# Optimization experiments

Measured on AMD Instinct MI355X. Metric: run time of the kernel, lower is better.

Reference implementation:

```python
import jax, jax.numpy as jnp
import numpy as np

N_HEADS = 8
STATE_TEMP = 0.5


def layer_norm(x, g, b, eps=1e-5):
    m = x.mean(-1, keepdims=True)
    v = ((x - m) ** 2).mean(-1, keepdims=True)
    return (x - m) / jnp.sqrt(v + eps) * g + b


def setup_inputs() -> dict:
    key = jax.random.key(0)
    ks = jax.random.split(key, 16)
    B, G, H, C, S, M, L = 2048, 10000, 256, 16, 32, 100, 3
    f32 = jnp.float32
    rn = lambda k, shape, scale: jax.random.normal(k, shape, f32) * scale
    return {
        'x': rn(ks[0], (B, G), 1.0),
        'enc_w1': rn(ks[1], (G, 2 * H), 1.0 / np.sqrt(G)),
        'enc_b1': jnp.zeros((2 * H,), f32),
        'enc_ln_g': jnp.ones((2 * H,), f32),
        'enc_ln_b': jnp.zeros((2 * H,), f32),
        'enc_w2': rn(ks[2], (2 * H, H), 1.0 / np.sqrt(2 * H)),
        'enc_b2': jnp.zeros((H,), f32),
        'mod_assign': rn(ks[3], (M, G), 1.0),
        'mod_inter': rn(ks[4], (M, M), 0.1) + jnp.eye(M, dtype=f32),
        'qkv_w': rn(ks[5], (L, H, 3 * H), 1.0 / np.sqrt(H)),
        'qkv_b': jnp.zeros((L, 3 * H), f32),
        'out_w': rn(ks[6], (L, H, H), 1.0 / np.sqrt(H)),
        'out_b': jnp.zeros((L, H), f32),
        'ln_g': jnp.ones((L, H), f32),
        'ln_b': jnp.zeros((L, H), f32),
        'prototypes': rn(ks[7], (S, H), 1.0),
        'clf_w1': rn(ks[8], (H, H // 2), 1.0 / np.sqrt(H)),
        'clf_b1': jnp.zeros((H // 2,), f32),
        'clf_w2': rn(ks[9], (H // 2, C), 1.0 / np.sqrt(H // 2)),
        'clf_b2': jnp.zeros((C,), f32),
        'marker_weights': jax.random.uniform(ks[10], (C, G), f32),
    }


def reference(x, enc_w1, enc_b1, enc_ln_g, enc_ln_b, enc_w2, enc_b2,
              mod_assign, mod_inter, qkv_w, qkv_b, out_w, out_b, ln_g, ln_b,
              prototypes, clf_w1, clf_b1, clf_w2, clf_b2, marker_weights):
    B = x.shape[0]
    Hd = enc_w2.shape[1]
    hd = Hd // N_HEADS
    # --- gene encoder (Linear -> LN -> ReLU -> Linear), dropout off (eval) ---
    h = jax.nn.relu(layer_norm(x @ enc_w1 + enc_b1, enc_ln_g, enc_ln_b))
    gene_features = h @ enc_w2 + enc_b2  # [B, Hd]
    # --- gene regulatory module (only sparsity_loss feeds the output dict) ---
    module_weights = jax.nn.softmax(mod_assign, axis=1)  # [M, G]
    sparsity_loss = jnp.mean(jnp.abs(module_weights)) * 0.01
    # --- stacked biological attention over seq_len N = 1 ---
    f = gene_features[:, None, :]  # [B, 1, Hd]
    for i in range(qkv_w.shape[0]):
        residual = f
        qkv = (f @ qkv_w[i] + qkv_b[i]).reshape(B, 1, 3, N_HEADS, hd)
        qkv = qkv.transpose(2, 0, 3, 1, 4)  # [3, B, nh, 1, hd]
        q, k, v = qkv[0], qkv[1], qkv[2]
        # N=1 != n_genes so the interaction-mask branch is skipped
        attn = jax.nn.softmax((q @ k.swapaxes(-2, -1)) * hd ** -0.5, axis=-1)
        o = (attn @ v).swapaxes(1, 2).reshape(B, 1, Hd)
        o = o @ out_w[i] + out_b[i]
        f = layer_norm(o + residual, ln_g[i], ln_b[i])
    feats = f[:, 0]  # [B, Hd]
    # --- soft assignment to cell-state prototypes via cosine similarity ---
    fn = jnp.linalg.norm(feats, axis=-1, keepdims=True)  # [B, 1]
    pn = jnp.linalg.norm(prototypes, axis=-1)            # [S]
    sim = (feats @ prototypes.T) / jnp.maximum(fn * pn[None, :], 1e-8)
    state_weights = jax.nn.softmax(sim / STATE_TEMP, axis=1)
    cell_states = state_weights @ prototypes  # [B, Hd]
    # --- classifier head ---
    logits = jax.nn.relu(cell_states @ clf_w1 + clf_b1) @ clf_w2 + clf_b2
    # --- eval-mode marker scores from buffer ---
    C, G = marker_weights.shape
    marker_scores = jnp.broadcast_to(marker_weights[None], (B, C, G))
    denom = jnp.maximum(jnp.sum(jnp.abs(marker_weights), axis=1, keepdims=True), 1e-12)
    marker_importance = marker_weights / denom
    return (logits, cell_states, sparsity_loss, marker_scores, marker_importance)
```

## Files before the change

### kernel.cpp

```cpp
#include <hip/hip_runtime.h>
#include <stdint.h>

#define GG 10000
#define H2 512
#define KP 10240
#define KCH 1280
#define KSTEPS 40

#define O_CS 32768L
#define O_SP 557056L
#define O_MS 557057L
#define O_MI 328237057L

typedef __attribute__((ext_vector_type(8))) short v8s;
typedef __attribute__((ext_vector_type(4))) float v4f;
typedef __attribute__((ext_vector_type(4))) unsigned short u16x4;
typedef __attribute__((ext_vector_type(8))) unsigned short u16x8;

__device__ __forceinline__ unsigned short bf16_rne(float f){
  unsigned u = __float_as_uint(f);
  u += 0x7fffu + ((u>>16)&1u);
  return (unsigned short)(u>>16);
}
__device__ __forceinline__ float bf16_f(unsigned short h){
  return __uint_as_float(((unsigned)h)<<16);
}

#define GL16(g,l) __builtin_amdgcn_global_load_lds( \
    (__attribute__((address_space(1))) void*)(uintptr_t)(g), \
    (__attribute__((address_space(3))) void*)(l), 16, 0, 0)

__global__ __launch_bounds__(256) void k_split_x(const float* __restrict__ x,
    unsigned short* __restrict__ xh){
  int idx = blockIdx.x*256 + threadIdx.x;
  int row = idx / (KP/4);
  int k = (idx - row*(KP/4))*4;
  float4 v = make_float4(0.f,0.f,0.f,0.f);
  if (k < GG) v = *(const float4*)(x + (long)row*GG + k);
  float c[4] = {v.x,v.y,v.z,v.w};
  u16x4 hv;
  #pragma unroll
  for (int j=0;j<4;j++) hv[j] = bf16_rne(c[j]);
  *(u16x4*)(xh + (long)row*KP + k) = hv;
}

__global__ __launch_bounds__(256) void k_split_w1t(const float* __restrict__ w1,
    unsigned short* __restrict__ wth, unsigned short* __restrict__ wtl){
  __shared__ unsigned T[64][65];
  int k0 = blockIdx.x*64, n0 = blockIdx.y*64;
  int tid = threadIdx.x;
  {
    int kr = tid>>2, nc = (tid&3)*16;
    int kk = k0 + kr;
    #pragma unroll
    for (int j=0;j<16;j+=4){
      float4 v = make_float4(0.f,0.f,0.f,0.f);
      if (kk < GG) v = *(const float4*)(w1 + (long)kk*H2 + n0 + nc + j);
      float c[4] = {v.x,v.y,v.z,v.w};
      #pragma unroll
      for (int jj=0;jj<4;jj++){
        unsigned short h = bf16_rne(c[jj]);
        unsigned short l = bf16_rne(c[jj] - bf16_f(h));
        T[kr][nc+j+jj] = (unsigned)h | ((unsigned)l<<16);
      }
    }
  }
  __syncthreads();
  {
    int n = tid>>2, kc = (tid&3)*16;
    u16x8 h0, h1, l0, l1;
    #pragma unroll
    for (int j=0;j<8;j++){
      unsigned a = T[kc+j][n];
      unsigned b = T[kc+8+j][n];
      h0[j] = (unsigned short)(a & 0xffffu); l0[j] = (unsigned short)(a>>16);
      h1[j] = (unsigned short)(b & 0xffffu); l1[j] = (unsigned short)(b>>16);
    }
    long off = (long)(n0+n)*KP + k0 + kc;
    *(u16x8*)(wth+off)   = h0; *(u16x8*)(wth+off+8) = h1;
    *(u16x8*)(wtl+off)   = l0; *(u16x8*)(wtl+off+8) = l1;
  }
}

__global__ __launch_bounds__(256) void k_gemm1(
    const unsigned short* __restrict__ xh,
    const unsigned short* __restrict__ wth, const unsigned short* __restrict__ wtl,
    float* __restrict__ pc){
  __shared__ unsigned short Ah[4096], Bh[4096], Bl[4096];
  const int tid = threadIdx.x;
  const int wid = tid>>6, lane = tid&63;
  const int bm = blockIdx.x, bn = blockIdx.y, kz = blockIdx.z;
  const int c0 = wid*2, c1 = c0+1;
  const int srow = lane>>2;
  const int sk8 = (lane&3)*8;
  const long kb0 = (long)kz*KCH + sk8;
  const long rA0 = (long)(bm*128 + c0*16 + srow)*KP + kb0;
  const long rA1 = (long)(bm*128 + c1*16 + srow)*KP + kb0;
  const long rB0 = (long)(bn*128 + c0*16 + srow)*KP + kb0;
  const long rB1 = (long)(bn*128 + c1*16 + srow)*KP + kb0;
  const unsigned short* pAh0 = xh + rA0;  const unsigned short* pAh1 = xh + rA1;
  const unsigned short* pBh0 = wth + rB0; const unsigned short* pBh1 = wth + rB1;
  const unsigned short* pBl0 = wtl + rB0; const unsigned short* pBl1 = wtl + rB1;
  unsigned short* dAh0 = &Ah[c0*512]; unsigned short* dAh1 = &Ah[c1*512];
  unsigned short* dBh0 = &Bh[c0*512]; unsigned short* dBh1 = &Bh[c1*512];
  unsigned short* dBl0 = &Bl[c0*512]; unsigned short* dBl1 = &Bl[c1*512];
  const int wr = wid>>1, wc = wid&1;
  const int fr = lane&15, fq = lane>>4;
  v4f acc[4][4];
  #pragma unroll
  for (int m=0;m<4;m++)
    #pragma unroll
    for (int n=0;n<4;n++){ v4f z = {0.f,0.f,0.f,0.f}; acc[m][n] = z; }

  for (int s=0; s<KSTEPS; ++s){
    GL16(pAh0, dAh0); GL16(pAh1, dAh1);
    GL16(pBh0, dBh0); GL16(pBh1, dBh1);
    GL16(pBl0, dBl0); GL16(pBl1, dBl1);
    pAh0 += 32; pAh1 += 32;
    pBh0 += 32; pBh1 += 32; pBl0 += 32; pBl1 += 32;
    __syncthreads();
    v8s ah[4], bh[4], bl[4];
    #pragma unroll
    for (int m=0;m<4;m++)
      ah[m] = *(const v8s*)&Ah[(wr*64 + m*16 + fr)*32 + fq*8];
    #pragma unroll
    for (int n=0;n<4;n++){
      int off = (wc*64 + n*16 + fr)*32 + fq*8;
      bh[n] = *(const v8s*)&Bh[off];
      bl[n] = *(const v8s*)&Bl[off];
    }
    #pragma unroll
    for (int m=0;m<4;m++)
      #pragma unroll
      for (int n=0;n<4;n++){
        acc[m][n] = __builtin_amdgcn_mfma_f32_16x16x32_bf16(ah[m], bh[n], acc[m][n], 0,0,0);
        acc[m][n] = __builtin_amdgcn_mfma_f32_16x16x32_bf16(ah[m], bl[n], acc[m][n], 0,0,0);
      }
    __syncthreads();
  }
  float* op = pc + (long)kz*(2048L*512L);
  #pragma unroll
  for (int m=0;m<4;m++){
    #pragma unroll
    for (int n=0;n<4;n++){
      int col = bn*128 + wc*64 + n*16 + fr;
      #pragma unroll
      for (int r=0;r<4;r++){
        int row = bm*128 + wr*64 + m*16 + fq*4 + r;
        op[(long)row*512 + col] = acc[m][n][r];
      }
    }
  }
}

__global__ __launch_bounds__(256) void k_reduce_ln(const float* __restrict__ pc,
    const float* __restrict__ b1, const float* __restrict__ g, const float* __restrict__ b,
    float* __restrict__ t1){
  __shared__ float red[8];
  int row = blockIdx.x, tid = threadIdx.x;
  long base = (long)row*512;
  float v0 = b1[tid], v1 = b1[tid+256];
  #pragma unroll
  for (int kz=0;kz<8;kz++){
    v0 += pc[(long)kz*1048576 + base + tid];
    v1 += pc[(long)kz*1048576 + base + tid + 256];
  }
  float s = v0+v1, q = v0*v0 + v1*v1;
  #pragma unroll
  for (int off=32; off; off>>=1){ s += __shfl_xor(s, off); q += __shfl_xor(q, off); }
  if ((tid&63)==0){ red[tid>>6] = s; red[4+(tid>>6)] = q; }
  __syncthreads();
  float sum = red[0]+red[1]+red[2]+red[3];
  float ssq = red[4]+red[5]+red[6]+red[7];
  float mean = sum*(1.f/512.f);
  float var  = ssq*(1.f/512.f) - mean*mean;
  float rstd = rsqrtf(var + 1e-5f);
  float r0 = (v0-mean)*rstd*g[tid]     + b[tid];
  float r1 = (v1-mean)*rstd*g[tid+256] + b[tid+256];
  t1[base+tid]     = fmaxf(r0, 0.f);
  t1[base+tid+256] = fmaxf(r1, 0.f);
}

__global__ __launch_bounds__(256) void k_gemm_f32(
    const float* __restrict__ A, int lda,
    const float* __restrict__ W, int ldw,
    const float* __restrict__ bias,
    float* __restrict__ C, int ldo, int K){
  __shared__ float As[64][36];
  __shared__ float WsT[64][36];
  const int tid = threadIdx.x;
  const int bx = blockIdx.x, by = blockIdx.y;
  const int tx = tid&15, ty = tid>>4;
  const int ar = tid>>2, ak = (tid&3)*8;
  const int wr2 = tid>>3, wc2 = (tid&7)*8;
  float acc[4][4];
  #pragma unroll
  for (int i=0;i<4;i++)
    #pragma unroll
    for (int j=0;j<4;j++) acc[i][j] = 0.f;
  for (int kb=0; kb<K; kb+=32){
    float4 a0 = *(const float4*)(A + (long)(bx*64+ar)*lda + kb + ak);
    float4 a1 = *(const float4*)(A + (long)(bx*64+ar)*lda + kb + ak + 4);
    float4 w0 = *(const float4*)(W + (long)(kb+wr2)*ldw + by*64 + wc2);
    float4 w1v= *(const float4*)(W + (long)(kb+wr2)*ldw + by*64 + wc2 + 4);
    __syncthreads();
    *(float4*)&As[ar][ak]   = a0;
    *(float4*)&As[ar][ak+4] = a1;
    float cw[8] = {w0.x,w0.y,w0.z,w0.w,w1v.x,w1v.y,w1v.z,w1v.w};
    #pragma unroll
    for (int jj=0;jj<8;jj++) WsT[wc2+jj][wr2] = cw[jj];
    __syncthreads();
    #pragma unroll
    for (int k4=0;k4<8;k4++){
      float4 av[4], wv[4];
      #pragma unroll
      for (int i=0;i<4;i++) av[i] = *(const float4*)&As[ty + i*16][k4*4];
      #pragma unroll
      for (int j=0;j<4;j++) wv[j] = *(const float4*)&WsT[tx + j*16][k4*4];
      #pragma unroll
      for (int i=0;i<4;i++)
        #pragma unroll
        for (int j=0;j<4;j++)
          acc[i][j] += av[i].x*wv[j].x + av[i].y*wv[j].y + av[i].z*wv[j].z + av[i].w*wv[j].w;
    }
  }
  #pragma unroll
  for (int i=0;i<4;i++){
    int r = bx*64 + ty + i*16;
    #pragma unroll
    for (int j=0;j<4;j++){
      int c = by*64 + tx + j*16;
      C[(long)r*ldo + c] = acc[i][j] + bias[c];
    }
  }
}

__global__ __launch_bounds__(256) void k_add_ln(const float* __restrict__ o,
    const float* __restrict__ res, const float* __restrict__ g, const float* __restrict__ b,
    float* __restrict__ fout){
  __shared__ float red[8];
  int row = blockIdx.x, tid = threadIdx.x;
  long base = (long)row*256;
  float x = o[base+tid] + res[base+tid];
  float s = x, q = x*x;
  #pragma unroll
  for (int off=32; off; off>>=1){ s += __shfl_xor(s, off); q += __shfl_xor(q, off); }
  if ((tid&63)==0){ red[tid>>6] = s; red[4+(tid>>6)] = q; }
  __syncthreads();
  float sum = red[0]+red[1]+red[2]+red[3];
  float ssq = red[4]+red[5]+red[6]+red[7];
  float mean = sum*(1.f/256.f);
  float var  = ssq*(1.f/256.f) - mean*mean;
  float rstd = rsqrtf(var + 1e-5f);
  fout[base+tid] = (x-mean)*rstd*g[tid] + b[tid];
}

__global__ __launch_bounds__(256) void k_head(const float* __restrict__ f,
    const float* __restrict__ protos, const float* __restrict__ w1, const float* __restrict__ b1,
    const float* __restrict__ w2, const float* __restrict__ b2,
    float* __restrict__ logits, float* __restrict__ cs_out){
  __shared__ float ff[256], csb[256], hid[128], simr[32], pnl[32], sw[32], red[8];
  int row = blockIdx.x, tid = threadIdx.x;
  float fv = f[(long)row*256 + tid];
  ff[tid] = fv;
  float s = fv*fv;
  #pragma unroll
  for (int off=32; off; off>>=1) s += __shfl_xor(s, off);
  if ((tid&63)==0) red[tid>>6] = s;
  __syncthreads();
  float fn = sqrtf(red[0]+red[1]+red[2]+red[3]);
  int p = tid>>3, e = tid&7;
  float d = 0.f, q = 0.f;
  for (int k=e*32; k<e*32+32; k++){ float pv = protos[p*256+k]; d += ff[k]*pv; q += pv*pv; }
  d += __shfl_xor(d,1); q += __shfl_xor(q,1);
  d += __shfl_xor(d,2); q += __shfl_xor(q,2);
  d += __shfl_xor(d,4); q += __shfl_xor(q,4);
  if (e==0){ simr[p] = d; pnl[p] = sqrtf(q); }
  __syncthreads();
  if (tid < 64){
    float z = (tid<32) ? (2.f*simr[tid]/fmaxf(fn*pnl[tid], 1e-8f)) : -3e38f;
    float m = z;
    #pragma unroll
    for (int off=16; off; off>>=1) m = fmaxf(m, __shfl_xor(m, off));
    float ev = (tid<32) ? expf(z - m) : 0.f;
    float sm = ev;
    #pragma unroll
    for (int off=16; off; off>>=1) sm += __shfl_xor(sm, off);
    if (tid<32) sw[tid] = ev/sm;
  }
  __syncthreads();
  float cs = 0.f;
  #pragma unroll 8
  for (int pp=0;pp<32;pp++) cs += sw[pp]*protos[pp*256+tid];
  cs_out[(long)row*256+tid] = cs;
  csb[tid] = cs;
  __syncthreads();
  if (tid<128){
    float hv = b1[tid];
    for (int k=0;k<256;k++) hv += csb[k]*w1[k*128+tid];
    hid[tid] = fmaxf(hv, 0.f);
  }
  __syncthreads();
  if (tid<16){
    float lv = b2[tid];
    for (int j=0;j<128;j++) lv += hid[j]*w2[j*16+tid];
    logits[(long)row*16+tid] = lv;
  }
}

__global__ void k_misc(float* __restrict__ out){
  if (threadIdx.x==0 && blockIdx.x==0) out[O_SP] = 0.01f/10000.0f;
}

__global__ __launch_bounds__(256) void k_fill_marker(const float* __restrict__ mw,
    float* __restrict__ out){
  int b = blockIdx.y;
  int t = blockIdx.x*256 + threadIdx.x;
  float* base = out + O_MS + (long)b*160000;
  if (t < 40000){
    int i = 4*t;
    float4 A  = *(const float4*)(mw + i);
    float4 Bv = (i+4 < 160000) ? *(const float4*)(mw + i + 4) : *(const float4*)(mw);
    float4 v = make_float4(A.w, Bv.x, Bv.y, Bv.z);
    *(float4*)(base + 3 + i) = v;
  }
  if (b==0 && t<3) base[t] = mw[t];
}

__global__ __launch_bounds__(256) void k_importance(const float* __restrict__ mw,
    float* __restrict__ out){
  __shared__ float red[4];
  int c = blockIdx.x, tid = threadIdx.x;
  float s = 0.f;
  for (int g0=tid; g0<10000; g0+=256) s += fabsf(mw[c*10000+g0]);
  #pragma unroll
  for (int off=32; off; off>>=1) s += __shfl_xor(s, off);
  if ((tid&63)==0) red[tid>>6] = s;
  __syncthreads();
  float inv = 1.f/fmaxf(red[0]+red[1]+red[2]+red[3], 1e-12f);
  for (int g0=tid; g0<10000; g0+=256)
    out[O_MI + (long)c*10000 + g0] = mw[c*10000+g0]*inv;
}

extern "C" void kernel_launch(void* const* d_in, const int* in_sizes, int n_in,
                              void* d_out, int out_size, void* d_ws, size_t ws_size,
                              hipStream_t stream){
  const float* x        = (const float*)d_in[0];
  const float* enc_w1   = (const float*)d_in[1];
  const float* enc_b1   = (const float*)d_in[2];
  const float* enc_ln_g = (const float*)d_in[3];
  const float* enc_ln_b = (const float*)d_in[4];
  const float* enc_w2   = (const float*)d_in[5];
  const float* enc_b2   = (const float*)d_in[6];
  const float* qkv_w    = (const float*)d_in[9];
  const float* qkv_b    = (const float*)d_in[10];
  const float* out_w    = (const float*)d_in[11];
  const float* out_b    = (const float*)d_in[12];
  const float* ln_g     = (const float*)d_in[13];
  const float* ln_b     = (const float*)d_in[14];
  const float* protos   = (const float*)d_in[15];
  const float* clf_w1   = (const float*)d_in[16];
  const float* clf_b1   = (const float*)d_in[17];
  const float* clf_w2   = (const float*)d_in[18];
  const float* clf_b2   = (const float*)d_in[19];
  const float* mw       = (const float*)d_in[20];
  float* out = (float*)d_out;

  char* scr = (char*)(((uintptr_t)d_out + O_MS*4 + 255) & ~(uintptr_t)255);
  unsigned short* xh  = (unsigned short*)(scr);
  unsigned short* wth = (unsigned short*)(scr + 83886080L);
  unsigned short* wtl = (unsigned short*)(scr + 94371840L);
  float* pc = (float*)(scr + 104857600L);
  float* t1 = (float*)(scr + 138412032L);
  float* f0 = (float*)(scr + 142606336L);
  float* f1 = (float*)(scr + 144703488L);
  float* vb = (float*)(scr + 146800640L);
  float* ob = (float*)(scr + 148897792L);

  k_split_x  <<<20480, 256, 0, stream>>>(x, xh);
  k_split_w1t<<<dim3(160, 8), 256, 0, stream>>>(enc_w1, wth, wtl);
  k_gemm1    <<<dim3(16, 4, 8), 256, 0, stream>>>(xh, wth, wtl, pc);
  k_reduce_ln<<<2048, 256, 0, stream>>>(pc, enc_b1, enc_ln_g, enc_ln_b, t1);
  k_gemm_f32 <<<dim3(32, 4), 256, 0, stream>>>(t1, 512, enc_w2, 256, enc_b2, f0, 256, 512);
  const float* fin = f0; float* fo = f1;
  for (int i=0;i<3;i++){
    k_gemm_f32<<<dim3(32,4), 256, 0, stream>>>(fin, 256, qkv_w + (long)i*196608 + 512, 768,
                                               qkv_b + i*768 + 512, vb, 256, 256);
    k_gemm_f32<<<dim3(32,4), 256, 0, stream>>>(vb, 256, out_w + (long)i*65536, 256,
                                               out_b + i*256, ob, 256, 256);
    k_add_ln  <<<2048, 256, 0, stream>>>(ob, fin, ln_g + i*256, ln_b + i*256, fo);
    const float* tmp = fo; fo = (float*)fin; fin = tmp;
  }
  k_head<<<2048, 256, 0, stream>>>(fin, protos, clf_w1, clf_b1, clf_w2, clf_b2,
                                   out, out + O_CS);
  k_misc<<<1, 64, 0, stream>>>(out);
  k_fill_marker<<<dim3(157, 2048), 256, 0, stream>>>(mw, out);
  k_importance <<<16, 256, 0, stream>>>(mw, out);
}
```

Measured before the change: 577.4 us.

## Double-buffer LDS in split-K bf16 GEMM, remap blocks per XCD, drop misc kernel

```diff
diff --git a/kernel.cpp b/kernel.cpp
--- a/kernel.cpp
+++ b/kernel.cpp
@@ -86,24 +86,28 @@
     const unsigned short* __restrict__ xh,
     const unsigned short* __restrict__ wth, const unsigned short* __restrict__ wtl,
     float* __restrict__ pc){
-  __shared__ unsigned short Ah[4096], Bh[4096], Bl[4096];
+  __shared__ unsigned short Ah[2][4096], Bh[2][4096], Bl[2][4096];
   const int tid = threadIdx.x;
   const int wid = tid>>6, lane = tid&63;
-  const int bm = blockIdx.x, bn = blockIdx.y, kz = blockIdx.z;
+  const int lid = blockIdx.x;
+  const int xcd = lid & 7;
+  const int q   = lid >> 3;
+  const int bm  = q & 15;
+  const int rr  = q >> 4;
+  const int r   = xcd + 8*rr;
+  const int bn  = r & 3;
+  const int kz  = r >> 2;
   const int c0 = wid*2, c1 = c0+1;
   const int srow = lane>>2;
   const int sk8 = (lane&3)*8;
   const long kb0 = (long)kz*KCH + sk8;
-  const long rA0 = (long)(bm*128 + c0*16 + srow)*KP + kb0;
-  const long rA1 = (long)(bm*128 + c1*16 + srow)*KP + kb0;
-  const long rB0 = (long)(bn*128 + c0*16 + srow)*KP + kb0;
-  const long rB1 = (long)(bn*128 + c1*16 + srow)*KP + kb0;
-  const unsigned short* pAh0 = xh + rA0;  const unsigned short* pAh1 = xh + rA1;
-  const unsigned short* pBh0 = wth + rB0; const unsigned short* pBh1 = wth + rB1;
-  const unsigned short* pBl0 = wtl + rB0; const unsigned short* pBl1 = wtl + rB1;
-  unsigned short* dAh0 = &Ah[c0*512]; unsigned short* dAh1 = &Ah[c1*512];
-  unsigned short* dBh0 = &Bh[c0*512]; unsigned short* dBh1 = &Bh[c1*512];
-  unsigned short* dBl0 = &Bl[c0*512]; unsigned short* dBl1 = &Bl[c1*512];
+  const unsigned short* pAh0 = xh  + (long)(bm*128 + c0*16 + srow)*KP + kb0;
+  const unsigned short* pAh1 = xh  + (long)(bm*128 + c1*16 + srow)*KP + kb0;
+  const unsigned short* pBh0 = wth + (long)(bn*128 + c0*16 + srow)*KP + kb0;
+  const unsigned short* pBh1 = wth + (long)(bn*128 + c1*16 + srow)*KP + kb0;
+  const unsigned short* pBl0 = wtl + (long)(bn*128 + c0*16 + srow)*KP + kb0;
+  const unsigned short* pBl1 = wtl + (long)(bn*128 + c1*16 + srow)*KP + kb0;
+  const int d0 = c0*512, d1 = c1*512;
   const int wr = wid>>1, wc = wid&1;
   const int fr = lane&15, fq = lane>>4;
   v4f acc[4][4];
@@ -112,22 +116,31 @@
     #pragma unroll
     for (int n=0;n<4;n++){ v4f z = {0.f,0.f,0.f,0.f}; acc[m][n] = z; }
 
+#define STAGE(d, s) do{ long o=(long)(s)*32; \
+    GL16(pAh0+o, &Ah[d][d0]); GL16(pAh1+o, &Ah[d][d1]); \
+    GL16(pBh0+o, &Bh[d][d0]); GL16(pBh1+o, &Bh[d][d1]); \
+    GL16(pBl0+o, &Bl[d][d0]); GL16(pBl1+o, &Bl[d][d1]); }while(0)
+
+  STAGE(0, 0);
+  int cur = 0;
   for (int s=0; s<KSTEPS; ++s){
-    GL16(pAh0, dAh0); GL16(pAh1, dAh1);
-    GL16(pBh0, dBh0); GL16(pBh1, dBh1);
-    GL16(pBl0, dBl0); GL16(pBl1, dBl1);
-    pAh0 += 32; pAh1 += 32;
-    pBh0 += 32; pBh1 += 32; pBl0 += 32; pBl1 += 32;
-    __syncthreads();
+    if (s+1 < KSTEPS){
+      STAGE(cur^1, s+1);
+      asm volatile("s_waitcnt vmcnt(6)" ::: "memory");
+    } else {
+      asm volatile("s_waitcnt vmcnt(0)" ::: "memory");
+    }
+    __builtin_amdgcn_s_barrier();
+    __builtin_amdgcn_sched_barrier(0);
     v8s ah[4], bh[4], bl[4];
     #pragma unroll
     for (int m=0;m<4;m++)
-      ah[m] = *(const v8s*)&Ah[(wr*64 + m*16 + fr)*32 + fq*8];
+      ah[m] = *(const v8s*)&Ah[cur][(wr*64 + m*16 + fr)*32 + fq*8];
     #pragma unroll
     for (int n=0;n<4;n++){
       int off = (wc*64 + n*16 + fr)*32 + fq*8;
-      bh[n] = *(const v8s*)&Bh[off];
-      bl[n] = *(const v8s*)&Bl[off];
+      bh[n] = *(const v8s*)&Bh[cur][off];
+      bl[n] = *(const v8s*)&Bl[cur][off];
     }
     #pragma unroll
     for (int m=0;m<4;m++)
@@ -136,8 +149,10 @@
         acc[m][n] = __builtin_amdgcn_mfma_f32_16x16x32_bf16(ah[m], bh[n], acc[m][n], 0,0,0);
         acc[m][n] = __builtin_amdgcn_mfma_f32_16x16x32_bf16(ah[m], bl[n], acc[m][n], 0,0,0);
       }
-    __syncthreads();
-  }
+    __builtin_amdgcn_s_barrier();
+    cur ^= 1;
+  }
+#undef STAGE
   float* op = pc + (long)kz*(2048L*512L);
   #pragma unroll
   for (int m=0;m<4;m++){
@@ -145,9 +160,9 @@
     for (int n=0;n<4;n++){
       int col = bn*128 + wc*64 + n*16 + fr;
       #pragma unroll
-      for (int r=0;r<4;r++){
-        int row = bm*128 + wr*64 + m*16 + fq*4 + r;
-        op[(long)row*512 + col] = acc[m][n][r];
+      for (int r2=0;r2<4;r2++){
+        int row = bm*128 + wr*64 + m*16 + fq*4 + r2;
+        op[(long)row*512 + col] = acc[m][n][r2];
       }
     }
   }
@@ -308,10 +323,6 @@
   }
 }
 
-__global__ void k_misc(float* __restrict__ out){
-  if (threadIdx.x==0 && blockIdx.x==0) out[O_SP] = 0.01f/10000.0f;
-}
-
 __global__ __launch_bounds__(256) void k_fill_marker(const float* __restrict__ mw,
     float* __restrict__ out){
   int b = blockIdx.y;
@@ -331,6 +342,7 @@
     float* __restrict__ out){
   __shared__ float red[4];
   int c = blockIdx.x, tid = threadIdx.x;
+  if (c==0 && tid==0) out[O_SP] = 0.01f/10000.0f;
   float s = 0.f;
   for (int g0=tid; g0<10000; g0+=256) s += fabsf(mw[c*10000+g0]);
   #pragma unroll
@@ -379,7 +391,7 @@
 
   k_split_x  <<<20480, 256, 0, stream>>>(x, xh);
   k_split_w1t<<<dim3(160, 8), 256, 0, stream>>>(enc_w1, wth, wtl);
-  k_gemm1    <<<dim3(16, 4, 8), 256, 0, stream>>>(xh, wth, wtl, pc);
+  k_gemm1    <<<512, 256, 0, stream>>>(xh, wth, wtl, pc);
   k_reduce_ln<<<2048, 256, 0, stream>>>(pc, enc_b1, enc_ln_g, enc_ln_b, t1);
   k_gemm_f32 <<<dim3(32, 4), 256, 0, stream>>>(t1, 512, enc_w2, 256, enc_b2, f0, 256, 512);
   const float* fin = f0; float* fo = f1;
@@ -393,7 +405,6 @@
   }
   k_head<<<2048, 256, 0, stream>>>(fin, protos, clf_w1, clf_b1, clf_w2, clf_b2,
                                    out, out + O_CS);
-  k_misc<<<1, 64, 0, stream>>>(out);
   k_fill_marker<<<dim3(157, 2048), 256, 0, stream>>>(mw, out);
   k_importance <<<16, 256, 0, stream>>>(mw, out);
 }
```

After: 583.9 us. About the same (+1.1%).

## Fold V and out-projection weights and fuse post-GEMM1 chain into one kernel

Applied to the files above, without the earlier changes.

```diff
diff --git a/kernel.cpp b/kernel.cpp
--- a/kernel.cpp
+++ b/kernel.cpp
@@ -29,6 +29,68 @@
 #define GL16(g,l) __builtin_amdgcn_global_load_lds( \
     (__attribute__((address_space(1))) void*)(uintptr_t)(g), \
     (__attribute__((address_space(3))) void*)(l), 16, 0, 0)
+
+__global__ __launch_bounds__(256) void k_prep0(const float* __restrict__ qkv_w,
+    const float* __restrict__ qkv_b, const float* __restrict__ out_w,
+    const float* __restrict__ out_b, float* __restrict__ Wc, float* __restrict__ bc){
+  __shared__ float As[64][36];
+  __shared__ float WsT[64][36];
+  const int bid = blockIdx.x, tid = threadIdx.x;
+  if (bid < 48){
+    const int z = bid>>4, bx = (bid&15)>>2, by = bid&3;
+    const float* A = qkv_w + (long)z*196608 + 512;
+    const float* W = out_w + (long)z*65536;
+    float* C = Wc + (long)z*65536;
+    const int tx = tid&15, ty = tid>>4;
+    const int ar = tid>>2, ak = (tid&3)*8;
+    const int wr2 = tid>>3, wc2 = (tid&7)*8;
+    float acc[4][4];
+    #pragma unroll
+    for (int i=0;i<4;i++)
+      #pragma unroll
+      for (int j=0;j<4;j++) acc[i][j] = 0.f;
+    for (int kb=0; kb<256; kb+=32){
+      float4 a0 = *(const float4*)(A + (long)(bx*64+ar)*768 + kb + ak);
+      float4 a1 = *(const float4*)(A + (long)(bx*64+ar)*768 + kb + ak + 4);
+      float4 w0 = *(const float4*)(W + (long)(kb+wr2)*256 + by*64 + wc2);
+      float4 w1v= *(const float4*)(W + (long)(kb+wr2)*256 + by*64 + wc2 + 4);
+      __syncthreads();
+      *(float4*)&As[ar][ak]   = a0;
+      *(float4*)&As[ar][ak+4] = a1;
+      float cw[8] = {w0.x,w0.y,w0.z,w0.w,w1v.x,w1v.y,w1v.z,w1v.w};
+      #pragma unroll
+      for (int jj=0;jj<8;jj++) WsT[wc2+jj][wr2] = cw[jj];
+      __syncthreads();
+      #pragma unroll
+      for (int k4=0;k4<8;k4++){
+        float4 av[4], wv[4];
+        #pragma unroll
+        for (int i=0;i<4;i++) av[i] = *(const float4*)&As[ty + i*16][k4*4];
+        #pragma unroll
+        for (int j=0;j<4;j++) wv[j] = *(const float4*)&WsT[tx + j*16][k4*4];
+        #pragma unroll
+        for (int i=0;i<4;i++)
+          #pragma unroll
+          for (int j=0;j<4;j++)
+            acc[i][j] += av[i].x*wv[j].x + av[i].y*wv[j].y + av[i].z*wv[j].z + av[i].w*wv[j].w;
+      }
+    }
+    #pragma unroll
+    for (int i=0;i<4;i++){
+      int r = bx*64 + ty + i*16;
+      #pragma unroll
+      for (int j=0;j<4;j++)
+        C[(long)r*256 + by*64 + tx + j*16] = acc[i][j];
+    }
+  } else {
+    int i = bid - 48;
+    float acc = out_b[i*256 + tid];
+    const float* wo = out_w + (long)i*65536;
+    const float* qb = qkv_b + i*768 + 512;
+    for (int j=0;j<256;j++) acc += qb[j]*wo[j*256+tid];
+    bc[i*256+tid] = acc;
+  }
+}
 
 __global__ __launch_bounds__(256) void k_split_x(const float* __restrict__ x,
     unsigned short* __restrict__ xh){
@@ -153,163 +215,177 @@
   }
 }
 
-__global__ __launch_bounds__(256) void k_reduce_ln(const float* __restrict__ pc,
-    const float* __restrict__ b1, const float* __restrict__ g, const float* __restrict__ b,
-    float* __restrict__ t1){
-  __shared__ float red[8];
-  int row = blockIdx.x, tid = threadIdx.x;
-  long base = (long)row*512;
-  float v0 = b1[tid], v1 = b1[tid+256];
+__global__ __launch_bounds__(256) void k_chain(
+    const float* __restrict__ pc, const float* __restrict__ b1,
+    const float* __restrict__ g1, const float* __restrict__ bb1,
+    const float* __restrict__ W2, const float* __restrict__ b2,
+    const float* __restrict__ Wc, const float* __restrict__ bc,
+    const float* __restrict__ lng, const float* __restrict__ lnb,
+    const float* __restrict__ protos,
+    const float* __restrict__ cw1, const float* __restrict__ cb1,
+    const float* __restrict__ cw2, const float* __restrict__ cb2,
+    float* __restrict__ logits, float* __restrict__ cs_out){
+  __shared__ float As[8][512];
+  __shared__ float Ws[32][256];
+  __shared__ float fs[8][256];
+  __shared__ float rs[8][4], rq[8][4];
+  __shared__ float simr[32], pnl[32], sw[32], red[4], hid[128];
+  const int tid = threadIdx.x;
+  const long r0 = (long)blockIdx.x*8;
+  const int w = tid>>6, lane = tid&63;
+
+  for (int r=0;r<8;r++){
+    long base = (r0+r)*512;
+    float v0 = b1[tid], v1 = b1[tid+256];
+    #pragma unroll
+    for (int kz=0;kz<8;kz++){
+      v0 += pc[(long)kz*1048576 + base + tid];
+      v1 += pc[(long)kz*1048576 + base + tid + 256];
+    }
+    float s = v0+v1, q = v0*v0 + v1*v1;
+    #pragma unroll
+    for (int off=32; off; off>>=1){ s += __shfl_xor(s,off); q += __shfl_xor(q,off); }
+    if (lane==0){ rs[r][w] = s; rq[r][w] = q; }
+    __syncthreads();
+    float sum = rs[r][0]+rs[r][1]+rs[r][2]+rs[r][3];
+    float ssq = rq[r][0]+rq[r][1]+rq[r][2]+rq[r][3];
+    float mean = sum*(1.f/512.f);
+    float var  = ssq*(1.f/512.f) - mean*mean;
+    float rstd = rsqrtf(var + 1e-5f);
+    As[r][tid]     = fmaxf((v0-mean)*rstd*g1[tid]     + bb1[tid],     0.f);
+    As[r][tid+256] = fmaxf((v1-mean)*rstd*g1[tid+256] + bb1[tid+256], 0.f);
+  }
+  __syncthreads();
+
+  {
+    float acc[8] = {0.f,0.f,0.f,0.f,0.f,0.f,0.f,0.f};
+    for (int c=0;c<16;c++){
+      #pragma unroll
+      for (int u=0;u<8;u++){
+        int p2 = u*256 + tid;
+        int j = p2>>6, c4 = (p2&63)*4;
+        *(float4*)&Ws[j][c4] = *(const float4*)(W2 + (long)(c*32+j)*256 + c4);
+      }
+      __syncthreads();
+      #pragma unroll
+      for (int j=0;j<32;j++){
+        float wv = Ws[j][tid];
+        #pragma unroll
+        for (int r=0;r<8;r++) acc[r] += As[r][c*32+j]*wv;
+      }
+      __syncthreads();
+    }
+    float bv = b2[tid];
+    #pragma unroll
+    for (int r=0;r<8;r++) fs[r][tid] = acc[r] + bv;
+  }
+  __syncthreads();
+
+  for (int i=0;i<3;i++){
+    float a2[8] = {0.f,0.f,0.f,0.f,0.f,0.f,0.f,0.f};
+    const float* Wi = Wc + (long)i*65536;
+    for (int c=0;c<8;c++){
+      #pragma unroll
+      for (int u=0;u<8;u++){
+        int p2 = u*256 + tid;
+        int j = p2>>6, c4 = (p2&63)*4;
+        *(float4*)&Ws[j][c4] = *(const float4*)(Wi + (long)(c*32+j)*256 + c4);
+      }
+      __syncthreads();
+      #pragma unroll
+      for (int j=0;j<32;j++){
+        float wv = Ws[j][tid];
+        #pragma unroll
+        for (int r=0;r<8;r++) a2[r] += fs[r][c*32+j]*wv;
+      }
+      __syncthreads();
+    }
+    float bcv = bc[i*256+tid], gv = lng[i*256+tid], bbv = lnb[i*256+tid];
+    float xv[8];
+    #pragma unroll
+    for (int r=0;r<8;r++) xv[r] = a2[r] + bcv + fs[r][tid];
+    #pragma unroll
+    for (int r=0;r<8;r++){
+      float s = xv[r], q = xv[r]*xv[r];
+      #pragma unroll
+      for (int off=32; off; off>>=1){ s += __shfl_xor(s,off); q += __shfl_xor(q,off); }
+      if (lane==0){ rs[r][w] = s; rq[r][w] = q; }
+    }
+    __syncthreads();
+    #pragma unroll
+    for (int r=0;r<8;r++){
+      float sum = rs[r][0]+rs[r][1]+rs[r][2]+rs[r][3];
+      float ssq = rq[r][0]+rq[r][1]+rq[r][2]+rq[r][3];
+      float mean = sum*(1.f/256.f);
+      float var  = ssq*(1.f/256.f) - mean*mean;
+      float rstd = rsqrtf(var + 1e-5f);
+      fs[r][tid] = (xv[r]-mean)*rstd*gv + bbv;
+    }
+    __syncthreads();
+  }
+
   #pragma unroll
-  for (int kz=0;kz<8;kz++){
-    v0 += pc[(long)kz*1048576 + base + tid];
-    v1 += pc[(long)kz*1048576 + base + tid + 256];
-  }
-  float s = v0+v1, q = v0*v0 + v1*v1;
-  #pragma unroll
-  for (int off=32; off; off>>=1){ s += __shfl_xor(s, off); q += __shfl_xor(q, off); }
-  if ((tid&63)==0){ red[tid>>6] = s; red[4+(tid>>6)] = q; }
-  __syncthreads();
-  float sum = red[0]+red[1]+red[2]+red[3];
-  float ssq = red[4]+red[5]+red[6]+red[7];
-  float mean = sum*(1.f/512.f);
-  float var  = ssq*(1.f/512.f) - mean*mean;
-  float rstd = rsqrtf(var + 1e-5f);
-  float r0 = (v0-mean)*rstd*g[tid]     + b[tid];
-  float r1 = (v1-mean)*rstd*g[tid+256] + b[tid+256];
-  t1[base+tid]     = fmaxf(r0, 0.f);
-  t1[base+tid+256] = fmaxf(r1, 0.f);
-}
-
-__global__ __launch_bounds__(256) void k_gemm_f32(
-    const float* __restrict__ A, int lda,
-    const float* __restrict__ W, int ldw,
-    const float* __restrict__ bias,
-    float* __restrict__ C, int ldo, int K){
-  __shared__ float As[64][36];
-  __shared__ float WsT[64][36];
-  const int tid = threadIdx.x;
-  const int bx = blockIdx.x, by = blockIdx.y;
-  const int tx = tid&15, ty = tid>>4;
-  const int ar = tid>>2, ak = (tid&3)*8;
-  const int wr2 = tid>>3, wc2 = (tid&7)*8;
-  float acc[4][4];
-  #pragma unroll
-  for (int i=0;i<4;i++)
-    #pragma unroll
-    for (int j=0;j<4;j++) acc[i][j] = 0.f;
-  for (int kb=0; kb<K; kb+=32){
-    float4 a0 = *(const float4*)(A + (long)(bx*64+ar)*lda + kb + ak);
-    float4 a1 = *(const float4*)(A + (long)(bx*64+ar)*lda + kb + ak + 4);
-    float4 w0 = *(const float4*)(W + (long)(kb+wr2)*ldw + by*64 + wc2);
-    float4 w1v= *(const float4*)(W + (long)(kb+wr2)*ldw + by*64 + wc2 + 4);
-    __syncthreads();
-    *(float4*)&As[ar][ak]   = a0;
-    *(float4*)&As[ar][ak+4] = a1;
-    float cw[8] = {w0.x,w0.y,w0.z,w0.w,w1v.x,w1v.y,w1v.z,w1v.w};
-    #pragma unroll
-    for (int jj=0;jj<8;jj++) WsT[wc2+jj][wr2] = cw[jj];
-    __syncthreads();
-    #pragma unroll
-    for (int k4=0;k4<8;k4++){
-      float4 av[4], wv[4];
-      #pragma unroll
-      for (int i=0;i<4;i++) av[i] = *(const float4*)&As[ty + i*16][k4*4];
-      #pragma unroll
-      for (int j=0;j<4;j++) wv[j] = *(const float4*)&WsT[tx + j*16][k4*4];
-      #pragma unroll
-      for (int i=0;i<4;i++)
-        #pragma unroll
-        for (int j=0;j<4;j++)
-          acc[i][j] += av[i].x*wv[j].x + av[i].y*wv[j].y + av[i].z*wv[j].z + av[i].w*wv[j].w;
-    }
-  }
-  #pragma unroll
-  for (int i=0;i<4;i++){
-    int r = bx*64 + ty + i*16;
-    #pragma unroll
-    for (int j=0;j<4;j++){
-      int c = by*64 + tx + j*16;
-      C[(long)r*ldo + c] = acc[i][j] + bias[c];
-    }
-  }
-}
-
-__global__ __launch_bounds__(256) void k_add_ln(const float* __restrict__ o,
-    const float* __restrict__ res, const float* __restrict__ g, const float* __restrict__ b,
-    float* __restrict__ fout){
-  __shared__ float red[8];
-  int row = blockIdx.x, tid = threadIdx.x;
-  long base = (long)row*256;
-  float x = o[base+tid] + res[base+tid];
-  float s = x, q = x*x;
-  #pragma unroll
-  for (int off=32; off; off>>=1){ s += __shfl_xor(s, off); q += __shfl_xor(q, off); }
-  if ((tid&63)==0){ red[tid>>6] = s; red[4+(tid>>6)] = q; }
-  __syncthreads();
-  float sum = red[0]+red[1]+red[2]+red[3];
-  float ssq = red[4]+red[5]+red[6]+red[7];
-  float mean = sum*(1.f/256.f);
-  float var  = ssq*(1.f/256.f) - mean*mean;
-  float rstd = rsqrtf(var + 1e-5f);
-  fout[base+tid] = (x-mean)*rstd*g[tid] + b[tid];
-}
-
-__global__ __launch_bounds__(256) void k_head(const float* __restrict__ f,
-    const float* __restrict__ protos, const float* __restrict__ w1, const float* __restrict__ b1,
-    const float* __restrict__ w2, const float* __restrict__ b2,
-    float* __restrict__ logits, float* __restrict__ cs_out){
-  __shared__ float ff[256], csb[256], hid[128], simr[32], pnl[32], sw[32], red[8];
-  int row = blockIdx.x, tid = threadIdx.x;
-  float fv = f[(long)row*256 + tid];
-  ff[tid] = fv;
-  float s = fv*fv;
-  #pragma unroll
-  for (int off=32; off; off>>=1) s += __shfl_xor(s, off);
-  if ((tid&63)==0) red[tid>>6] = s;
-  __syncthreads();
-  float fn = sqrtf(red[0]+red[1]+red[2]+red[3]);
-  int p = tid>>3, e = tid&7;
-  float d = 0.f, q = 0.f;
-  for (int k=e*32; k<e*32+32; k++){ float pv = protos[p*256+k]; d += ff[k]*pv; q += pv*pv; }
-  d += __shfl_xor(d,1); q += __shfl_xor(q,1);
-  d += __shfl_xor(d,2); q += __shfl_xor(q,2);
-  d += __shfl_xor(d,4); q += __shfl_xor(q,4);
-  if (e==0){ simr[p] = d; pnl[p] = sqrtf(q); }
-  __syncthreads();
-  if (tid < 64){
-    float z = (tid<32) ? (2.f*simr[tid]/fmaxf(fn*pnl[tid], 1e-8f)) : -3e38f;
-    float m = z;
-    #pragma unroll
-    for (int off=16; off; off>>=1) m = fmaxf(m, __shfl_xor(m, off));
-    float ev = (tid<32) ? expf(z - m) : 0.f;
-    float sm = ev;
-    #pragma unroll
-    for (int off=16; off; off>>=1) sm += __shfl_xor(sm, off);
-    if (tid<32) sw[tid] = ev/sm;
-  }
-  __syncthreads();
-  float cs = 0.f;
-  #pragma unroll 8
-  for (int pp=0;pp<32;pp++) cs += sw[pp]*protos[pp*256+tid];
-  cs_out[(long)row*256+tid] = cs;
-  csb[tid] = cs;
-  __syncthreads();
-  if (tid<128){
-    float hv = b1[tid];
-    for (int k=0;k<256;k++) hv += csb[k]*w1[k*128+tid];
-    hid[tid] = fmaxf(hv, 0.f);
-  }
-  __syncthreads();
-  if (tid<16){
-    float lv = b2[tid];
-    for (int j=0;j<128;j++) lv += hid[j]*w2[j*16+tid];
-    logits[(long)row*16+tid] = lv;
-  }
-}
-
-__global__ void k_misc(float* __restrict__ out){
-  if (threadIdx.x==0 && blockIdx.x==0) out[O_SP] = 0.01f/10000.0f;
+  for (int u=0;u<8;u++){
+    int p2 = u*256 + tid;
+    int j = p2>>6, c4 = (p2&63)*4;
+    *(float4*)&Ws[j][c4] = *(const float4*)(protos + (long)j*256 + c4);
+  }
+  __syncthreads();
+  {
+    int p = tid>>3, e = tid&7;
+    float q = 0.f;
+    for (int k=e*32; k<e*32+32; k++){ float pv = Ws[p][k]; q += pv*pv; }
+    q += __shfl_xor(q,1); q += __shfl_xor(q,2); q += __shfl_xor(q,4);
+    if (e==0) pnl[p] = sqrtf(q);
+  }
+  __syncthreads();
+  for (int r=0;r<8;r++){
+    float fv = fs[r][tid];
+    float s = fv*fv;
+    #pragma unroll
+    for (int off=32; off; off>>=1) s += __shfl_xor(s,off);
+    if (lane==0) red[w] = s;
+    __syncthreads();
+    float fn = sqrtf(red[0]+red[1]+red[2]+red[3]);
+    {
+      int p = tid>>3, e = tid&7;
+      float d = 0.f;
+      for (int k=e*32; k<e*32+32; k++) d += fs[r][k]*Ws[p][k];
+      d += __shfl_xor(d,1); d += __shfl_xor(d,2); d += __shfl_xor(d,4);
+      if (e==0) simr[p] = d;
+    }
+    __syncthreads();
+    if (tid < 64){
+      float z = (tid<32) ? (2.f*simr[tid]/fmaxf(fn*pnl[tid], 1e-8f)) : -3e38f;
+      float m = z;
+      #pragma unroll
+      for (int off=16; off; off>>=1) m = fmaxf(m, __shfl_xor(m, off));
+      float ev = (tid<32) ? expf(z - m) : 0.f;
+      float sm = ev;
+      #pragma unroll
+      for (int off=16; off; off>>=1) sm += __shfl_xor(sm, off);
+      if (tid<32) sw[tid] = ev/sm;
+    }
+    __syncthreads();
+    float cs = 0.f;
+    #pragma unroll 8
+    for (int pp=0;pp<32;pp++) cs += sw[pp]*Ws[pp][tid];
+    cs_out[(r0+r)*256 + tid] = cs;
+    As[0][tid] = cs;
+    __syncthreads();
+    if (tid<128){
+      float hv = cb1[tid];
+      for (int k=0;k<256;k++) hv += As[0][k]*cw1[k*128+tid];
+      hid[tid] = fmaxf(hv, 0.f);
+    }
+    __syncthreads();
+    if (tid<16){
+      float lv = cb2[tid];
+      for (int j=0;j<128;j++) lv += hid[j]*cw2[j*16+tid];
+      logits[(r0+r)*16 + tid] = lv;
+    }
+    __syncthreads();
+  }
 }
 
 __global__ __launch_bounds__(256) void k_fill_marker(const float* __restrict__ mw,
@@ -331,6 +407,7 @@
     float* __restrict__ out){
   __shared__ float red[4];
   int c = blockIdx.x, tid = threadIdx.x;
+  if (c==0 && tid==0) out[O_SP] = 0.01f/10000.0f;
   float s = 0.f;
   for (int g0=tid; g0<10000; g0+=256) s += fabsf(mw[c*10000+g0]);
   #pragma unroll
@@ -371,29 +448,17 @@
   unsigned short* wth = (unsigned short*)(scr + 83886080L);
   unsigned short* wtl = (unsigned short*)(scr + 94371840L);
   float* pc = (float*)(scr + 104857600L);
-  float* t1 = (float*)(scr + 138412032L);
-  float* f0 = (float*)(scr + 142606336L);
-  float* f1 = (float*)(scr + 144703488L);
-  float* vb = (float*)(scr + 146800640L);
-  float* ob = (float*)(scr + 148897792L);
-
+  float* Wc = (float*)(scr + 138412032L);
+  float* bc = (float*)(scr + 139198464L);
+
+  k_prep0    <<<51, 256, 0, stream>>>(qkv_w, qkv_b, out_w, out_b, Wc, bc);
   k_split_x  <<<20480, 256, 0, stream>>>(x, xh);
   k_split_w1t<<<dim3(160, 8), 256, 0, stream>>>(enc_w1, wth, wtl);
   k_gemm1    <<<dim3(16, 4, 8), 256, 0, stream>>>(xh, wth, wtl, pc);
-  k_reduce_ln<<<2048, 256, 0, stream>>>(pc, enc_b1, enc_ln_g, enc_ln_b, t1);
-  k_gemm_f32 <<<dim3(32, 4), 256, 0, stream>>>(t1, 512, enc_w2, 256, enc_b2, f0, 256, 512);
-  const float* fin = f0; float* fo = f1;
-  for (int i=0;i<3;i++){
-    k_gemm_f32<<<dim3(32,4), 256, 0, stream>>>(fin, 256, qkv_w + (long)i*196608 + 512, 768,
-                                               qkv_b + i*768 + 512, vb, 256, 256);
-    k_gemm_f32<<<dim3(32,4), 256, 0, stream>>>(vb, 256, out_w + (long)i*65536, 256,
-                                               out_b + i*256, ob, 256, 256);
-    k_add_ln  <<<2048, 256, 0, stream>>>(ob, fin, ln_g + i*256, ln_b + i*256, fo);
-    const float* tmp = fo; fo = (float*)fin; fin = tmp;
-  }
-  k_head<<<2048, 256, 0, stream>>>(fin, protos, clf_w1, clf_b1, clf_w2, clf_b2,
-                                   out, out + O_CS);
-  k_misc<<<1, 64, 0, stream>>>(out);
+  k_chain    <<<256, 256, 0, stream>>>(pc, enc_b1, enc_ln_g, enc_ln_b,
+                                       enc_w2, enc_b2, Wc, bc, ln_g, ln_b,
+                                       protos, clf_w1, clf_b1, clf_w2, clf_b2,
+                                       out, out + O_CS);
   k_fill_marker<<<dim3(157, 2048), 256, 0, stream>>>(mw, out);
   k_importance <<<16, 256, 0, stream>>>(mw, out);
 }
```

Result: slower. 653.0 us (+13.1%).
